# Optimization experiments

Measured on AMD Instinct MI355X. Metric: run time of the kernel, lower is better.

Reference implementation:

```python
import jax, jax.numpy as jnp
import numpy as np

HID = 128
NLAYERS = 8
LAT = 32
DIM_IN = 63 + 15 + LAT  # pe(xyz,L=10)=3+60, pe(shift,L=2)=3+12, latent=32 -> 110


def _pe(x, L):
    # NeRF positional encoding, include_input=True, freq-major [sin3,cos3] per freq
    freqs = (2.0 ** jnp.arange(L)).astype(x.dtype)
    xf = x[..., None, :] * freqs[:, None]                      # [..., L, 3]
    sc = jnp.concatenate([jnp.sin(xf), jnp.cos(xf)], axis=-1)  # [..., L, 6]
    return jnp.concatenate([x, sc.reshape(*x.shape[:-1], 6 * L)], axis=-1)


def setup_inputs() -> dict:
    key = jax.random.key(0)
    ks = jax.random.split(key, 24)
    B, P, V = 2, 32768, 5023
    d = {}
    d["pts"] = jax.random.normal(ks[0], (B, P, 3), jnp.float32)
    d["deformed_mesh_pts"] = jax.random.normal(ks[1], (B, V, 3), jnp.float32)
    d["cano_verts"] = jax.random.normal(ks[2], (1, V, 3), jnp.float32)
    d["motion_latent"] = jax.random.normal(ks[3], (B, P, LAT), jnp.float32)
    for i in range(NLAYERS):
        fin = DIM_IN if i == 0 else (DIM_IN + HID if i == NLAYERS // 2 else HID)
        d[f"w{i}"] = jax.random.normal(ks[4 + i], (HID, fin), jnp.float32) / np.sqrt(fin).astype(np.float32)
        d[f"b{i}"] = jnp.zeros((HID,), jnp.float32)
    d["w_out"] = jax.random.normal(ks[20], (3, HID), jnp.float32) * 0.01
    d["b_out"] = jnp.zeros((3,), jnp.float32)
    return d


def reference(pts, deformed_mesh_pts, cano_verts, motion_latent,
              w0, b0, w1, b1, w2, b2, w3, b3, w4, b4, w5, b5, w6, b6, w7, b7,
              w_out, b_out):
    # mesh-guided shift per vertex
    mesh_shift = cano_verts - deformed_mesh_pts                 # [B,V,3]
    # point-to-point NN search (squared euclidean cdist + argmin)
    d2 = ((pts ** 2).sum(-1)[:, :, None]
          + (deformed_mesh_pts ** 2).sum(-1)[:, None, :]
          - 2.0 * jnp.einsum('bpc,bvc->bpv', pts, deformed_mesh_pts))  # [B,P,V]
    d2 = jnp.maximum(d2, 0.0)
    idx = jnp.argmin(d2, axis=-1)                               # [B,P]
    dist = jnp.min(d2, axis=-1)                                 # [B,P]
    weight = jnp.exp(-dist)[..., None]                          # 1/exp(dist)
    gidx = jnp.broadcast_to(idx[:, :, None], idx.shape + (3,))
    gshift = jnp.take_along_axis(mesh_shift, gidx, axis=1) * weight  # [B,P,3]
    # deformation MLP with skip connection at layer 4
    initial = jnp.concatenate([_pe(pts, 10), _pe(gshift, 2), motion_latent], axis=-1)
    ws = [w0, w1, w2, w3, w4, w5, w6, w7]
    bs = [b0, b1, b2, b3, b4, b5, b6, b7]
    x = initial
    last_feat = x
    for i in range(NLAYERS):
        inp = jnp.concatenate([initial, x], axis=-1) if i == NLAYERS // 2 else x
        x = inp @ ws[i].T + bs[i]
        last_feat = x  # pre-activation feature (out_feat_ls[-1])
        x = jax.nn.relu(x)
    mlp_shift = x @ w_out.T + b_out                             # [B,P,3]
    pts_shifts = gshift + mlp_shift
    return pts + pts_shifts, last_feat
```

## Files before the change

### kernel.cpp

```cpp
#include <hip/hip_runtime.h>
#include <math.h>

typedef unsigned short ushort_t;
typedef unsigned int   uint_t;
typedef __attribute__((ext_vector_type(8)))  short bf16x8;
typedef __attribute__((ext_vector_type(16))) float f32x16;

#define NPTS   65536
#define NV     5023
#define NVP    5120
#define NTILE  160
#define HTILE  80
#define LATD   32
#define KF     110
#define FSTR   112
#define MARGIN 1.5e-2f

union U4 { uint_t u[4]; bf16x8 v; };

__device__ __forceinline__ ushort_t f2bf(float f) {
  union { float f; unsigned u; } x; x.f = f;
  unsigned r = x.u + 0x7fffu + ((x.u >> 16) & 1u);
  return (ushort_t)(r >> 16);
}
__device__ __forceinline__ float bf2f(ushort_t u) {
  union { unsigned u; float f; } x; x.u = ((unsigned)u) << 16;
  return x.f;
}
__device__ __forceinline__ uint_t packsplit(float v) {
  const ushort_t h = f2bf(v);
  const ushort_t l = f2bf(v - bf2f(h));
  return (uint_t)h | ((uint_t)l << 16);
}

__device__ __forceinline__ void dbl_step(float& s, float& c) {
  const float t = s * c;
  const float cn = fmaf(-2.f * s, s, 1.f);
  s = t + t;
  c = cn;
}

__global__ __launch_bounds__(256) void k_prep(
    const float* __restrict__ dm,
    const float* __restrict__ w0, const float* __restrict__ w1,
    const float* __restrict__ w2, const float* __restrict__ w3,
    const float* __restrict__ w4, const float* __restrict__ w5,
    const float* __restrict__ w6, const float* __restrict__ w7,
    ushort_t* __restrict__ wsWh, ushort_t* __restrict__ wsWl,
    ushort_t* __restrict__ aFF, ushort_t* __restrict__ aFH,
    float4* __restrict__ vq)
{
  const int e = blockIdx.x * 256 + threadIdx.x;
  {
    const int p = e >> 14, local = e & 16383;
    const int j   = local & 7;
    const int lh  = (local >> 3) & 1;
    const int l31 = (local >> 4) & 31;
    const int tn  = (local >> 9) & 3;
    const int ks  = (local >> 11) & 7;
    const int n = tn*32 + l31;
    const int k = ks*16 + lh*8 + j;
    float v;
    if (p == 0)      v = (k < KF) ? w0[n*110 + k] : 0.f;
    else if (p == 1) v = w1[n*128 + k];
    else if (p == 2) v = w2[n*128 + k];
    else if (p == 3) v = w3[n*128 + k];
    else if (p == 4) v = (k < KF) ? w4[n*238 + k] : 0.f;
    else if (p == 5) v = w4[n*238 + KF + k];
    else if (p == 6) v = w5[n*128 + k];
    else if (p == 7) v = w6[n*128 + k];
    else             v = w7[n*128 + k];
    const ushort_t h = f2bf(v);
    wsWh[e] = h;
    wsWl[e] = f2bf(v - bf2f(h));
  }
  if (e < 2*NVP) {
    const int b = (e >= NVP) ? 1 : 0;
    const int v = e - b*NVP;
    const float* __restrict__ dmb = dm + b*NV*3;
    float x = 0.f, y = 0.f, z = 0.f, wv = 3.0e38f;
    if (v < NV) {
      x = dmb[v*3+0]; y = dmb[v*3+1]; z = dmb[v*3+2];
      wv = fmaf(x,x, fmaf(y,y, z*z));
    }
    const ushort_t hx = f2bf(x),  hy = f2bf(y),  hz = f2bf(z),  hw = f2bf(wv);
    const ushort_t lx = f2bf(x - bf2f(hx)), ly = f2bf(y - bf2f(hy));
    const ushort_t lz = f2bf(z - bf2f(hz)), lw = f2bf(wv - bf2f(hw));
    U4 F, H;
    F.u[0] = (uint_t)hx | ((uint_t)hy << 16);
    F.u[1] = (uint_t)hz | ((uint_t)hw << 16);
    F.u[2] = (uint_t)lx | ((uint_t)ly << 16);
    F.u[3] = (uint_t)lz | ((uint_t)lw << 16);
    H.u[0] = F.u[0]; H.u[1] = F.u[1]; H.u[2] = 0; H.u[3] = 0;
    *(bf16x8*)(aFF + (size_t)e*8) = F.v;
    *(bf16x8*)(aFH + (size_t)e*8) = H.v;
    vq[e] = make_float4(x, y, z, wv);
  }
}

__device__ __forceinline__ float min16(const f32x16& d) {
  const float t0 = fminf(fminf(d[0],d[1]),   fminf(d[2],d[3]));
  const float t1 = fminf(fminf(d[4],d[5]),   fminf(d[6],d[7]));
  const float t2 = fminf(fminf(d[8],d[9]),   fminf(d[10],d[11]));
  const float t3 = fminf(fminf(d[12],d[13]), fminf(d[14],d[15]));
  return fminf(fminf(t0,t1), fminf(t2,t3));
}

__global__ __launch_bounds__(256, 4) void k_nnfeat(
    const float* __restrict__ pts, const float* __restrict__ dm,
    const float* __restrict__ cano, const float* __restrict__ lat,
    const ushort_t* __restrict__ aFF, const ushort_t* __restrict__ aFH,
    const float4* __restrict__ vq,
    uint_t* __restrict__ feat, float* __restrict__ base3)
{
  __shared__ float sMin[2][64];
  __shared__ float sDh[2][64];
  __shared__ int   sIh[2][64];

  const int tid = threadIdx.x;
  const int lane = tid & 63, w = tid >> 6;
  const int l31 = lane & 31, lh = lane >> 5;
  const int half = w & 1, pg = w >> 1;
  const int g0 = blockIdx.x * 64;
  const int b  = blockIdx.x >> 9;
  const int pt = g0 + pg*32 + l31;
  const int pidx = pg*32 + l31;

  const float px = pts[pt*3+0], py = pts[pt*3+1], pz = pts[pt*3+2];
  const float p2 = fmaf(px,px, fmaf(py,py, pz*pz));

  const float tpx = -2.f*px, tpy = -2.f*py, tpz = -2.f*pz;
  const ushort_t hpx = f2bf(tpx), hpy = f2bf(tpy), hpz = f2bf(tpz);
  const ushort_t lpx = f2bf(tpx - bf2f(hpx));
  const ushort_t lpy = f2bf(tpy - bf2f(hpy));
  const ushort_t lpz = f2bf(tpz - bf2f(hpz));
  U4 Bh, Bl;
  Bh.u[0] = (uint_t)hpx | ((uint_t)hpy << 16);
  Bh.u[1] = (uint_t)hpz | (0x3F80u << 16);
  Bh.u[2] = Bh.u[0]; Bh.u[3] = Bh.u[1];
  Bl.u[0] = (uint_t)lpx | ((uint_t)lpy << 16);
  Bl.u[1] = (uint_t)lpz;
  Bl.u[2] = 0; Bl.u[3] = 0;
  const bf16x8 bfrag = lh ? Bl.v : Bh.v;

  const ushort_t* __restrict__ aBase = (lh ? aFH : aFF)
      + (size_t)b * NVP * 8 + (size_t)half * HTILE * 32 * 8;
  const float4*   __restrict__ vqb   = vq + (size_t)b * NVP;
  const int vho = half * HTILE * 32;

  const f32x16 zacc = (f32x16)(0.f);

  float gmin = 3.0e38f;
  bf16x8 ap0, ap1, ap2, ap3, an0, an1, an2, an3;
  ap0 = *(const bf16x8*)(aBase + (size_t)(0*32 + l31)*8);
  ap1 = *(const bf16x8*)(aBase + (size_t)(1*32 + l31)*8);
  ap2 = *(const bf16x8*)(aBase + (size_t)(2*32 + l31)*8);
  ap3 = *(const bf16x8*)(aBase + (size_t)(3*32 + l31)*8);
  #pragma unroll 2
  for (int tb = 0; tb < HTILE/4; ++tb) {
    const int t0 = tb*4;
    if (tb + 1 < HTILE/4) {
      an0 = *(const bf16x8*)(aBase + (size_t)((t0+4)*32 + l31)*8);
      an1 = *(const bf16x8*)(aBase + (size_t)((t0+5)*32 + l31)*8);
      an2 = *(const bf16x8*)(aBase + (size_t)((t0+6)*32 + l31)*8);
      an3 = *(const bf16x8*)(aBase + (size_t)((t0+7)*32 + l31)*8);
    }
    const f32x16 d0 = __builtin_amdgcn_mfma_f32_32x32x16_bf16(ap0, bfrag, zacc, 0,0,0);
    const f32x16 d1 = __builtin_amdgcn_mfma_f32_32x32x16_bf16(ap1, bfrag, zacc, 0,0,0);
    const f32x16 d2 = __builtin_amdgcn_mfma_f32_32x32x16_bf16(ap2, bfrag, zacc, 0,0,0);
    const f32x16 d3 = __builtin_amdgcn_mfma_f32_32x32x16_bf16(ap3, bfrag, zacc, 0,0,0);
    const float m0 = min16(d0), m1 = min16(d1), m2 = min16(d2), m3 = min16(d3);
    gmin = fminf(gmin, fminf(fminf(m0,m1), fminf(m2,m3)));
    ap0 = an0; ap1 = an1; ap2 = an2; ap3 = an3;
  }
  gmin = fminf(gmin, __shfl_xor(gmin, 32, 64));
  if (lh == 0) sMin[half][pidx] = gmin;
  __syncthreads();
  const float thr = fminf(sMin[0][pidx], sMin[1][pidx]) + MARGIN;

  float bs = 3.4e38f; int bi = 0;
  ap0 = *(const bf16x8*)(aBase + (size_t)(0*32 + l31)*8);
  ap1 = *(const bf16x8*)(aBase + (size_t)(1*32 + l31)*8);
  ap2 = *(const bf16x8*)(aBase + (size_t)(2*32 + l31)*8);
  ap3 = *(const bf16x8*)(aBase + (size_t)(3*32 + l31)*8);
  #pragma unroll 1
  for (int tb = 0; tb < HTILE/4; ++tb) {
    const int t0 = tb*4;
    if (tb + 1 < HTILE/4) {
      an0 = *(const bf16x8*)(aBase + (size_t)((t0+4)*32 + l31)*8);
      an1 = *(const bf16x8*)(aBase + (size_t)((t0+5)*32 + l31)*8);
      an2 = *(const bf16x8*)(aBase + (size_t)((t0+6)*32 + l31)*8);
      an3 = *(const bf16x8*)(aBase + (size_t)((t0+7)*32 + l31)*8);
    }
    f32x16 dd[4];
    dd[0] = __builtin_amdgcn_mfma_f32_32x32x16_bf16(ap0, bfrag, zacc, 0,0,0);
    dd[1] = __builtin_amdgcn_mfma_f32_32x32x16_bf16(ap1, bfrag, zacc, 0,0,0);
    dd[2] = __builtin_amdgcn_mfma_f32_32x32x16_bf16(ap2, bfrag, zacc, 0,0,0);
    dd[3] = __builtin_amdgcn_mfma_f32_32x32x16_bf16(ap3, bfrag, zacc, 0,0,0);
    #pragma unroll
    for (int i = 0; i < 4; ++i) {
      const f32x16 d = dd[i];
      float q4[4];
      q4[0] = fminf(fminf(d[0],d[1]),   fminf(d[2],d[3]));
      q4[1] = fminf(fminf(d[4],d[5]),   fminf(d[6],d[7]));
      q4[2] = fminf(fminf(d[8],d[9]),   fminf(d[10],d[11]));
      q4[3] = fminf(fminf(d[12],d[13]), fminf(d[14],d[15]));
      const float tm = fminf(fminf(q4[0],q4[1]), fminf(q4[2],q4[3]));
      if (tm <= thr) {
        const int t = t0 + i;
        #pragma unroll
        for (int q = 0; q < 4; ++q) {
          if (q4[q] <= thr) {
            #pragma unroll
            for (int rr = 0; rr < 4; ++rr) {
              const int r = q*4 + rr;
              if (d[r] <= thr) {
                const int row = (r & 3) + 8*(r >> 2) + 4*lh;
                const int v = vho + t*32 + row;
                const float4 qv = vqb[v];
                const float dot = fmaf(px, qv.x, fmaf(py, qv.y, pz*qv.z));
                float d2 = fmaf(-2.f, dot, p2 + qv.w);
                d2 = fmaxf(d2, 0.f);
                if (d2 < bs || (d2 == bs && v < bi)) { bs = d2; bi = v; }
              }
            }
          }
        }
      }
    }
    ap0 = an0; ap1 = an1; ap2 = an2; ap3 = an3;
  }
  {
    const float ob = __shfl_xor(bs, 32, 64);
    const int   oi = __shfl_xor(bi, 32, 64);
    if (ob < bs || (ob == bs && oi < bi)) { bs = ob; bi = oi; }
  }
  if (lh == 0) { sDh[half][pidx] = bs; sIh[half][pidx] = bi; }
  __syncthreads();

  const int p = tid & 63, slice = tid >> 6;
  const int g = g0 + p;
  float wd = sDh[0][p]; int wi = sIh[0][p];
  {
    const float od = sDh[1][p]; const int oi = sIh[1][p];
    if (od < wd || (od == wd && oi < wi)) { wd = od; wi = oi; }
  }
  const float* __restrict__ dmb = dm + b * NV * 3;

  const float qx = pts[g*3+0], qy = pts[g*3+1], qz = pts[g*3+2];
  const float wgt = expf(-wd);
  const float sx = (cano[wi*3+0] - dmb[wi*3+0]) * wgt;
  const float sy = (cano[wi*3+1] - dmb[wi*3+1]) * wgt;
  const float sz = (cano[wi*3+2] - dmb[wi*3+2]) * wgt;

  uint_t* __restrict__ fr = feat + (size_t)g * FSTR;

  if (slice == 0) {
    base3[g*3+0] = qx + sx; base3[g*3+1] = qy + sy; base3[g*3+2] = qz + sz;
    fr[0] = packsplit(qx); fr[1] = packsplit(qy); fr[2] = packsplit(qz);
    float s0,c0,s1,c1,s2,c2;
    sincosf(qx,&s0,&c0); sincosf(qy,&s1,&c1); sincosf(qz,&s2,&c2);
    #pragma unroll
    for (int f = 0; f < 3; ++f) {
      const int k = 3 + 6*f;
      fr[k+0]=packsplit(s0); fr[k+1]=packsplit(s1); fr[k+2]=packsplit(s2);
      fr[k+3]=packsplit(c0); fr[k+4]=packsplit(c1); fr[k+5]=packsplit(c2);
      if (f < 2) { dbl_step(s0,c0); dbl_step(s1,c1); dbl_step(s2,c2); }
    }
    fr[110] = 0; fr[111] = 0;
  } else if (slice == 1) {
    float s0,c0,s1,c1,s2,c2;
    sincosf(qx*8.f,&s0,&c0); sincosf(qy*8.f,&s1,&c1); sincosf(qz*8.f,&s2,&c2);
    #pragma unroll
    for (int f = 3; f < 7; ++f) {
      const int k = 3 + 6*f;
      fr[k+0]=packsplit(s0); fr[k+1]=packsplit(s1); fr[k+2]=packsplit(s2);
      fr[k+3]=packsplit(c0); fr[k+4]=packsplit(c1); fr[k+5]=packsplit(c2);
      if (f < 6) { dbl_step(s0,c0); dbl_step(s1,c1); dbl_step(s2,c2); }
    }
  } else if (slice == 2) {
    float s0,c0,s1,c1,s2,c2;
    sincosf(qx*128.f,&s0,&c0); sincosf(qy*128.f,&s1,&c1); sincosf(qz*128.f,&s2,&c2);
    #pragma unroll
    for (int f = 7; f < 10; ++f) {
      const int k = 3 + 6*f;
      fr[k+0]=packsplit(s0); fr[k+1]=packsplit(s1); fr[k+2]=packsplit(s2);
      fr[k+3]=packsplit(c0); fr[k+4]=packsplit(c1); fr[k+5]=packsplit(c2);
      if (f < 9) { dbl_step(s0,c0); dbl_step(s1,c1); dbl_step(s2,c2); }
    }
    #pragma unroll
    for (int j = 0; j < 16; ++j) fr[78+j] = packsplit(lat[g*LATD + j]);
  } else {
    fr[63]=packsplit(sx); fr[64]=packsplit(sy); fr[65]=packsplit(sz);
    float s0,c0,s1,c1,s2,c2;
    sincosf(sx,&s0,&c0); sincosf(sy,&s1,&c1); sincosf(sz,&s2,&c2);
    #pragma unroll
    for (int f = 0; f < 2; ++f) {
      const int k = 66 + 6*f;
      fr[k+0]=packsplit(s0); fr[k+1]=packsplit(s1); fr[k+2]=packsplit(s2);
      fr[k+3]=packsplit(c0); fr[k+4]=packsplit(c1); fr[k+5]=packsplit(c2);
      if (f < 1) { dbl_step(s0,c0); dbl_step(s1,c1); dbl_step(s2,c2); }
    }
    #pragma unroll
    for (int j = 16; j < 32; ++j) fr[78+j] = packsplit(lat[g*LATD + j]);
  }
}


__device__ __forceinline__ void zero4(f32x16 (&a)[4]) {
  #pragma unroll
  for (int i = 0; i < 4; ++i) a[i] = (f32x16)(0.f);
}

__device__ __forceinline__ void load_feat_frags(
    const uint_t* __restrict__ fr, bf16x8 (&Xh)[8], bf16x8 (&Xl)[8], int lh)
{
  #pragma unroll
  for (int ks = 0; ks < 7; ++ks) {
    const int k0 = ks*16 + lh*8;
    const uint4 ua = *(const uint4*)(fr + k0);
    const uint4 ub = *(const uint4*)(fr + k0 + 4);
    U4 H, L;
    H.u[0] = (ua.x & 0xffffu) | (ua.y << 16);
    H.u[1] = (ua.z & 0xffffu) | (ua.w << 16);
    H.u[2] = (ub.x & 0xffffu) | (ub.y << 16);
    H.u[3] = (ub.z & 0xffffu) | (ub.w << 16);
    L.u[0] = (ua.x >> 16) | (ua.y & 0xffff0000u);
    L.u[1] = (ua.z >> 16) | (ua.w & 0xffff0000u);
    L.u[2] = (ub.x >> 16) | (ub.y & 0xffff0000u);
    L.u[3] = (ub.z >> 16) | (ub.w & 0xffff0000u);
    Xh[ks] = H.v; Xl[ks] = L.v;
  }
}

__device__ __forceinline__ void load_slab(bf16x8 (&wh)[4], bf16x8 (&wl)[4],
    const ushort_t* __restrict__ Wh, const ushort_t* __restrict__ Wl,
    int ks, int l31, int lh)
{
  const int lo = l31*16 + lh*8;
  #pragma unroll
  for (int tn = 0; tn < 4; ++tn) {
    const int off = (ks*4 + tn)*512 + lo;
    wh[tn] = *(const bf16x8*)(Wh + off);
    wl[tn] = *(const bf16x8*)(Wl + off);
  }
}

__device__ __forceinline__ void mfma_slab(f32x16 (&acc)[4],
    const bf16x8 (&wh)[4], const bf16x8 (&wl)[4],
    const bf16x8& xh, const bf16x8& xl)
{
  #pragma unroll
  for (int tn = 0; tn < 4; ++tn) {
    acc[tn] = __builtin_amdgcn_mfma_f32_32x32x16_bf16(wh[tn], xh, acc[tn], 0,0,0);
    acc[tn] = __builtin_amdgcn_mfma_f32_32x32x16_bf16(wl[tn], xh, acc[tn], 0,0,0);
    acc[tn] = __builtin_amdgcn_mfma_f32_32x32x16_bf16(wh[tn], xl, acc[tn], 0,0,0);
  }
}

template<int NKS, bool TAIL>
__device__ __forceinline__ void run_panel(f32x16 (&acc)[4],
    const ushort_t* __restrict__ Wh, const ushort_t* __restrict__ Wl,
    const ushort_t* __restrict__ WhN, const ushort_t* __restrict__ WlN,
    bf16x8 (&wbh)[2][4], bf16x8 (&wbl)[2][4],
    const bf16x8 (&Xh)[8], const bf16x8 (&Xl)[8], int l31, int lh)
{
  #pragma unroll
  for (int ks = 0; ks < NKS; ++ks) {
    const int b = ks & 1;
    mfma_slab(acc, wbh[b], wbl[b], Xh[ks], Xl[ks]);
    if (ks + 2 < NKS) {
      load_slab(wbh[b], wbl[b], Wh, Wl, ks + 2, l31, lh);
    } else if (TAIL) {
      load_slab(wbh[b], wbl[b], WhN, WlN, ks & 1, l31, lh);
    }
  }
}

__device__ __forceinline__ void bias_relu(f32x16 (&acc)[4],
    const float* __restrict__ bias, int lh)
{
  #pragma unroll
  for (int tn = 0; tn < 4; ++tn)
    #pragma unroll
    for (int b = 0; b < 4; ++b) {
      const float4 b4 = *(const float4*)(bias + tn*32 + 8*b + 4*lh);
      acc[tn][4*b+0] = fmaxf(acc[tn][4*b+0] + b4.x, 0.f);
      acc[tn][4*b+1] = fmaxf(acc[tn][4*b+1] + b4.y, 0.f);
      acc[tn][4*b+2] = fmaxf(acc[tn][4*b+2] + b4.z, 0.f);
      acc[tn][4*b+3] = fmaxf(acc[tn][4*b+3] + b4.w, 0.f);
    }
}

__device__ __forceinline__ void build_frags(const f32x16 (&acc)[4],
    bf16x8 (&Xh)[8], bf16x8 (&Xl)[8], int lh)
{
  #pragma unroll
  for (int ks = 0; ks < 8; ++ks) {
    const int tn = ks >> 1;
    const int rb = 8*(ks & 1);
    const float f0 = acc[tn][rb+0], f1 = acc[tn][rb+1];
    const float f2 = acc[tn][rb+2], f3 = acc[tn][rb+3];
    const float f4 = acc[tn][rb+4], f5 = acc[tn][rb+5];
    const float f6 = acc[tn][rb+6], f7 = acc[tn][rb+7];
    const ushort_t h0=f2bf(f0), h1=f2bf(f1), h2=f2bf(f2), h3=f2bf(f3);
    const ushort_t h4=f2bf(f4), h5=f2bf(f5), h6=f2bf(f6), h7=f2bf(f7);
    const uint_t hA0 = (uint_t)h0 | ((uint_t)h1 << 16);
    const uint_t hA1 = (uint_t)h2 | ((uint_t)h3 << 16);
    const uint_t hB0 = (uint_t)h4 | ((uint_t)h5 << 16);
    const uint_t hB1 = (uint_t)h6 | ((uint_t)h7 << 16);
    const uint_t lA0 = (uint_t)f2bf(f0 - bf2f(h0)) | ((uint_t)f2bf(f1 - bf2f(h1)) << 16);
    const uint_t lA1 = (uint_t)f2bf(f2 - bf2f(h2)) | ((uint_t)f2bf(f3 - bf2f(h3)) << 16);
    const uint_t lB0 = (uint_t)f2bf(f4 - bf2f(h4)) | ((uint_t)f2bf(f5 - bf2f(h5)) << 16);
    const uint_t lB1 = (uint_t)f2bf(f6 - bf2f(h6)) | ((uint_t)f2bf(f7 - bf2f(h7)) << 16);
    const uint_t sh0 = lh ? hA0 : hB0, sh1 = lh ? hA1 : hB1;
    const uint_t sl0 = lh ? lA0 : lB0, sl1 = lh ? lA1 : lB1;
    const uint_t rh0 = __shfl_xor(sh0, 32, 64), rh1 = __shfl_xor(sh1, 32, 64);
    const uint_t rl0 = __shfl_xor(sl0, 32, 64), rl1 = __shfl_xor(sl1, 32, 64);
    U4 H, L;
    H.u[0] = lh ? rh0 : hA0;  H.u[1] = lh ? rh1 : hA1;
    H.u[2] = lh ? hB0 : rh0;  H.u[3] = lh ? hB1 : rh1;
    L.u[0] = lh ? rl0 : lA0;  L.u[1] = lh ? rl1 : lA1;
    L.u[2] = lh ? lB0 : rl0;  L.u[3] = lh ? lB1 : rl1;
    Xh[ks] = H.v; Xl[ks] = L.v;
  }
}

__global__ __launch_bounds__(256, 2) void k_mlp(
    const uint_t* __restrict__ feat, const float* __restrict__ base3,
    const ushort_t* __restrict__ wsWh, const ushort_t* __restrict__ wsWl,
    const float* __restrict__ b0, const float* __restrict__ b1,
    const float* __restrict__ b2, const float* __restrict__ b3,
    const float* __restrict__ b4, const float* __restrict__ b5,
    const float* __restrict__ b6, const float* __restrict__ b7,
    const float* __restrict__ w_out, const float* __restrict__ b_out,
    float* __restrict__ out)
{
  __shared__ __align__(16) float sF[4][32*132];
  __shared__ __align__(16) float sB[8*128 + 384 + 4];

  const int tid  = threadIdx.x;
  const int lane = tid & 63, wid = tid >> 6;
  const int l31 = lane & 31, lh = lane >> 5;
  const int p0 = blockIdx.x * 128 + wid * 32;

  {
    const float* bsp[8] = {b0,b1,b2,b3,b4,b5,b6,b7};
    if (tid < 128) {
      #pragma unroll
      for (int l = 0; l < 8; ++l) sB[l*128 + tid] = bsp[l][tid];
    }
    for (int i = tid; i < 384; i += 256) sB[1024 + i] = w_out[i];
    if (tid < 3) sB[1408 + tid] = b_out[tid];
  }

  const uint_t* __restrict__ fr = feat + (size_t)(p0 + l31) * FSTR;

  bf16x8 Xh[8], Xl[8];
  bf16x8 wbh[2][4], wbl[2][4];
  f32x16 acc[4];

  load_slab(wbh[0], wbl[0], wsWh, wsWl, 0, l31, lh);
  load_slab(wbh[1], wbl[1], wsWh, wsWl, 1, l31, lh);
  load_feat_frags(fr, Xh, Xl, lh);
  __syncthreads();

  zero4(acc);
  run_panel<7,true>(acc, wsWh + 0*16384, wsWl + 0*16384,
                         wsWh + 1*16384, wsWl + 1*16384, wbh, wbl, Xh, Xl, l31, lh);
  bias_relu(acc, sB + 0*128, lh);
  build_frags(acc, Xh, Xl, lh);

  zero4(acc);
  run_panel<8,true>(acc, wsWh + 1*16384, wsWl + 1*16384,
                         wsWh + 2*16384, wsWl + 2*16384, wbh, wbl, Xh, Xl, l31, lh);
  bias_relu(acc, sB + 1*128, lh);
  build_frags(acc, Xh, Xl, lh);

  zero4(acc);
  run_panel<8,true>(acc, wsWh + 2*16384, wsWl + 2*16384,
                         wsWh + 3*16384, wsWl + 3*16384, wbh, wbl, Xh, Xl, l31, lh);
  bias_relu(acc, sB + 2*128, lh);
  build_frags(acc, Xh, Xl, lh);

  zero4(acc);
  run_panel<8,true>(acc, wsWh + 3*16384, wsWl + 3*16384,
                         wsWh + 5*16384, wsWl + 5*16384, wbh, wbl, Xh, Xl, l31, lh);
  bias_relu(acc, sB + 3*128, lh);
  build_frags(acc, Xh, Xl, lh);

  zero4(acc);
  run_panel<8,true>(acc, wsWh + 5*16384, wsWl + 5*16384,
                         wsWh + 4*16384, wsWl + 4*16384, wbh, wbl, Xh, Xl, l31, lh);
  load_feat_frags(fr, Xh, Xl, lh);
  run_panel<7,true>(acc, wsWh + 4*16384, wsWl + 4*16384,
                         wsWh + 6*16384, wsWl + 6*16384, wbh, wbl, Xh, Xl, l31, lh);
  bias_relu(acc, sB + 4*128, lh);
  build_frags(acc, Xh, Xl, lh);

  zero4(acc);
  run_panel<8,true>(acc, wsWh + 6*16384, wsWl + 6*16384,
                         wsWh + 7*16384, wsWl + 7*16384, wbh, wbl, Xh, Xl, l31, lh);
  bias_relu(acc, sB + 5*128, lh);
  build_frags(acc, Xh, Xl, lh);

  zero4(acc);
  run_panel<8,true>(acc, wsWh + 7*16384, wsWl + 7*16384,
                         wsWh + 8*16384, wsWl + 8*16384, wbh, wbl, Xh, Xl, l31, lh);
  bias_relu(acc, sB + 6*128, lh);
  build_frags(acc, Xh, Xl, lh);

  zero4(acc);
  run_panel<8,false>(acc, wsWh + 8*16384, wsWl + 8*16384,
                          (const ushort_t*)0, (const ushort_t*)0, wbh, wbl, Xh, Xl, l31, lh);

  float* __restrict__ sFw = &sF[wid][0];
  #pragma unroll
  for (int tn = 0; tn < 4; ++tn)
    #pragma unroll
    for (int b = 0; b < 4; ++b) {
      const int n0 = tn*32 + 8*b + 4*lh;
      const float4 bv = *(const float4*)(sB + 7*128 + n0);
      const float v0 = acc[tn][4*b+0] + bv.x;
      const float v1 = acc[tn][4*b+1] + bv.y;
      const float v2 = acc[tn][4*b+2] + bv.z;
      const float v3 = acc[tn][4*b+3] + bv.w;
      *(float4*)(sFw + l31*132 + n0) = make_float4(v0, v1, v2, v3);
      acc[tn][4*b+0] = fmaxf(v0, 0.f);
      acc[tn][4*b+1] = fmaxf(v1, 0.f);
      acc[tn][4*b+2] = fmaxf(v2, 0.f);
      acc[tn][4*b+3] = fmaxf(v3, 0.f);
    }

  asm volatile("s_waitcnt lgkmcnt(0)" ::: "memory");
  __builtin_amdgcn_sched_barrier(0);

  float* __restrict__ out1 = out + (size_t)NPTS * 3;
  #pragma unroll
  for (int i = 0; i < 16; ++i) {
    const int idx = i*64 + lane;
    const int p = idx >> 5, q = idx & 31;
    const float4 v = *(const float4*)(sFw + p*132 + q*4);
    *(float4*)(out1 + (size_t)(p0 + p)*128 + q*4) = v;
  }

  float dotc[3];
  #pragma unroll
  for (int c = 0; c < 3; ++c) {
    float a = 0.f;
    #pragma unroll
    for (int tn = 0; tn < 4; ++tn)
      #pragma unroll
      for (int b = 0; b < 4; ++b) {
        const int n0 = tn*32 + 8*b + 4*lh;
        const float4 w4 = *(const float4*)(sB + 1024 + c*128 + n0);
        a = fmaf(acc[tn][4*b+0], w4.x, a);
        a = fmaf(acc[tn][4*b+1], w4.y, a);
        a = fmaf(acc[tn][4*b+2], w4.z, a);
        a = fmaf(acc[tn][4*b+3], w4.w, a);
      }
    a += __shfl_xor(a, 32, 64);
    dotc[c] = a;
  }
  if (lh == 0) {
    const int g = p0 + l31;
    #pragma unroll
    for (int c = 0; c < 3; ++c)
      out[g*3 + c] = base3[g*3 + c] + dotc[c] + sB[1408 + c];
  }
}

extern "C" void kernel_launch(void* const* d_in, const int* in_sizes, int n_in,
                              void* d_out, int out_size, void* d_ws, size_t ws_size,
                              hipStream_t stream)
{
  const float* pts  = (const float*)d_in[0];
  const float* dm   = (const float*)d_in[1];
  const float* cano = (const float*)d_in[2];
  const float* lat  = (const float*)d_in[3];
  const float* w[8]; const float* b[8];
  for (int i = 0; i < 8; ++i) {
    w[i] = (const float*)d_in[4 + 2*i];
    b[i] = (const float*)d_in[5 + 2*i];
  }
  const float* w_out = (const float*)d_in[20];
  const float* b_out = (const float*)d_in[21];
  float* out = (float*)d_out;

  uint_t*   feat  = (uint_t*)d_ws;
  float*    base3 = (float*)((char*)d_ws + (size_t)NPTS*FSTR*4);
  ushort_t* wsWh  = (ushort_t*)((char*)base3 + (size_t)NPTS*3*4);
  ushort_t* wsWl  = wsWh + 147456;
  ushort_t* aFF   = wsWl + 147456;
  ushort_t* aFH   = aFF + 2*NVP*8;
  float4*   vq    = (float4*)(aFH + 2*NVP*8);

  k_prep<<<576, 256, 0, stream>>>(dm,
      w[0],w[1],w[2],w[3],w[4],w[5],w[6],w[7], wsWh, wsWl, aFF, aFH, vq);
  k_nnfeat<<<1024, 256, 0, stream>>>(pts, dm, cano, lat, aFF, aFH, vq, feat, base3);
  k_mlp<<<NPTS/128, 256, 0, stream>>>(feat, base3, wsWh, wsWl,
      b[0],b[1],b[2],b[3],b[4],b[5],b[6],b[7], w_out, b_out, out);
}
```

Baseline: 232.1 us.

## Split NN vertex scan across four waves per 32-point block, doubling grid

Each block now handles 32 points instead of 64, with its four waves each scanning a quarter of the vertex tiles instead of two waves per half. Partial minima and argmins are merged through shared memory over four slots. The feature-writing epilogue is spread over eight 32-thread slices, with latent packing split into four slices. Launch bounds ask for 8 blocks per CU and the grid doubles to 2048. The aim is shorter per-wave serial scans and more parallelism, at the cost of more block overhead and more pressure on registers to reach the higher occupancy target.

```diff
diff --git a/kernel.cpp b/kernel.cpp
--- a/kernel.cpp
+++ b/kernel.cpp
@@ -10,7 +10,7 @@
 #define NV     5023
 #define NVP    5120
 #define NTILE  160
-#define HTILE  80
+#define QTILE  40
 #define LATD   32
 #define KF     110
 #define FSTR   112
@@ -106,25 +106,23 @@
   return fminf(fminf(t0,t1), fminf(t2,t3));
 }
 
-__global__ __launch_bounds__(256, 4) void k_nnfeat(
+__global__ __launch_bounds__(256, 8) void k_nnfeat(
     const float* __restrict__ pts, const float* __restrict__ dm,
     const float* __restrict__ cano, const float* __restrict__ lat,
     const ushort_t* __restrict__ aFF, const ushort_t* __restrict__ aFH,
     const float4* __restrict__ vq,
     uint_t* __restrict__ feat, float* __restrict__ base3)
 {
-  __shared__ float sMin[2][64];
-  __shared__ float sDh[2][64];
-  __shared__ int   sIh[2][64];
+  __shared__ float sMin[4][32];
+  __shared__ float sDh[4][32];
+  __shared__ int   sIh[4][32];
 
   const int tid = threadIdx.x;
   const int lane = tid & 63, w = tid >> 6;
   const int l31 = lane & 31, lh = lane >> 5;
-  const int half = w & 1, pg = w >> 1;
-  const int g0 = blockIdx.x * 64;
-  const int b  = blockIdx.x >> 9;
-  const int pt = g0 + pg*32 + l31;
-  const int pidx = pg*32 + l31;
+  const int g0 = blockIdx.x * 32;
+  const int b  = blockIdx.x >> 10;
+  const int pt = g0 + l31;
 
   const float px = pts[pt*3+0], py = pts[pt*3+1], pz = pts[pt*3+2];
   const float p2 = fmaf(px,px, fmaf(py,py, pz*pz));
@@ -144,9 +142,9 @@
   const bf16x8 bfrag = lh ? Bl.v : Bh.v;
 
   const ushort_t* __restrict__ aBase = (lh ? aFH : aFF)
-      + (size_t)b * NVP * 8 + (size_t)half * HTILE * 32 * 8;
+      + (size_t)b * NVP * 8 + (size_t)w * QTILE * 32 * 8;
   const float4*   __restrict__ vqb   = vq + (size_t)b * NVP;
-  const int vho = half * HTILE * 32;
+  const int vho = w * QTILE * 32;
 
   const f32x16 zacc = (f32x16)(0.f);
 
@@ -157,9 +155,9 @@
   ap2 = *(const bf16x8*)(aBase + (size_t)(2*32 + l31)*8);
   ap3 = *(const bf16x8*)(aBase + (size_t)(3*32 + l31)*8);
   #pragma unroll 2
-  for (int tb = 0; tb < HTILE/4; ++tb) {
+  for (int tb = 0; tb < QTILE/4; ++tb) {
     const int t0 = tb*4;
-    if (tb + 1 < HTILE/4) {
+    if (tb + 1 < QTILE/4) {
       an0 = *(const bf16x8*)(aBase + (size_t)((t0+4)*32 + l31)*8);
       an1 = *(const bf16x8*)(aBase + (size_t)((t0+5)*32 + l31)*8);
       an2 = *(const bf16x8*)(aBase + (size_t)((t0+6)*32 + l31)*8);
@@ -174,9 +172,10 @@
     ap0 = an0; ap1 = an1; ap2 = an2; ap3 = an3;
   }
   gmin = fminf(gmin, __shfl_xor(gmin, 32, 64));
-  if (lh == 0) sMin[half][pidx] = gmin;
+  if (lane < 32) sMin[w][l31] = gmin;
   __syncthreads();
-  const float thr = fminf(sMin[0][pidx], sMin[1][pidx]) + MARGIN;
+  const float thr = fminf(fminf(sMin[0][l31], sMin[1][l31]),
+                          fminf(sMin[2][l31], sMin[3][l31])) + MARGIN;
 
   float bs = 3.4e38f; int bi = 0;
   ap0 = *(const bf16x8*)(aBase + (size_t)(0*32 + l31)*8);
@@ -184,9 +183,9 @@
   ap2 = *(const bf16x8*)(aBase + (size_t)(2*32 + l31)*8);
   ap3 = *(const bf16x8*)(aBase + (size_t)(3*32 + l31)*8);
   #pragma unroll 1
-  for (int tb = 0; tb < HTILE/4; ++tb) {
+  for (int tb = 0; tb < QTILE/4; ++tb) {
     const int t0 = tb*4;
-    if (tb + 1 < HTILE/4) {
+    if (tb + 1 < QTILE/4) {
       an0 = *(const bf16x8*)(aBase + (size_t)((t0+4)*32 + l31)*8);
       an1 = *(const bf16x8*)(aBase + (size_t)((t0+5)*32 + l31)*8);
       an2 = *(const bf16x8*)(aBase + (size_t)((t0+6)*32 + l31)*8);
@@ -235,14 +234,15 @@
     const int   oi = __shfl_xor(bi, 32, 64);
     if (ob < bs || (ob == bs && oi < bi)) { bs = ob; bi = oi; }
   }
-  if (lh == 0) { sDh[half][pidx] = bs; sIh[half][pidx] = bi; }
+  if (lane < 32) { sDh[w][l31] = bs; sIh[w][l31] = bi; }
   __syncthreads();
 
-  const int p = tid & 63, slice = tid >> 6;
+  const int p = tid & 31, slice = tid >> 5;
   const int g = g0 + p;
   float wd = sDh[0][p]; int wi = sIh[0][p];
-  {
-    const float od = sDh[1][p]; const int oi = sIh[1][p];
+  #pragma unroll
+  for (int qq = 1; qq < 4; ++qq) {
+    const float od = sDh[qq][p]; const int oi = sIh[qq][p];
     if (od < wd || (od == wd && oi < wi)) { wd = od; wi = oi; }
   }
   const float* __restrict__ dmb = dm + b * NV * 3;
@@ -267,7 +267,6 @@
       fr[k+3]=packsplit(c0); fr[k+4]=packsplit(c1); fr[k+5]=packsplit(c2);
       if (f < 2) { dbl_step(s0,c0); dbl_step(s1,c1); dbl_step(s2,c2); }
     }
-    fr[110] = 0; fr[111] = 0;
   } else if (slice == 1) {
     float s0,c0,s1,c1,s2,c2;
     sincosf(qx*8.f,&s0,&c0); sincosf(qy*8.f,&s1,&c1); sincosf(qz*8.f,&s2,&c2);
@@ -288,9 +287,7 @@
       fr[k+3]=packsplit(c0); fr[k+4]=packsplit(c1); fr[k+5]=packsplit(c2);
       if (f < 9) { dbl_step(s0,c0); dbl_step(s1,c1); dbl_step(s2,c2); }
     }
-    #pragma unroll
-    for (int j = 0; j < 16; ++j) fr[78+j] = packsplit(lat[g*LATD + j]);
-  } else {
+  } else if (slice == 3) {
     fr[63]=packsplit(sx); fr[64]=packsplit(sy); fr[65]=packsplit(sz);
     float s0,c0,s1,c1,s2,c2;
     sincosf(sx,&s0,&c0); sincosf(sy,&s1,&c1); sincosf(sz,&s2,&c2);
@@ -301,8 +298,11 @@
       fr[k+3]=packsplit(c0); fr[k+4]=packsplit(c1); fr[k+5]=packsplit(c2);
       if (f < 1) { dbl_step(s0,c0); dbl_step(s1,c1); dbl_step(s2,c2); }
     }
-    #pragma unroll
-    for (int j = 16; j < 32; ++j) fr[78+j] = packsplit(lat[g*LATD + j]);
+    fr[110] = 0; fr[111] = 0;
+  } else {
+    const int j0 = (slice - 4) * 8;
+    #pragma unroll
+    for (int j = 0; j < 8; ++j) fr[78 + j0 + j] = packsplit(lat[g*LATD + j0 + j]);
   }
 }
 
@@ -597,7 +597,7 @@
 
   k_prep<<<576, 256, 0, stream>>>(dm,
       w[0],w[1],w[2],w[3],w[4],w[5],w[6],w[7], wsWh, wsWl, aFF, aFH, vq);
-  k_nnfeat<<<1024, 256, 0, stream>>>(pts, dm, cano, lat, aFF, aFH, vq, feat, base3);
+  k_nnfeat<<<2048, 256, 0, stream>>>(pts, dm, cano, lat, aFF, aFH, vq, feat, base3);
   k_mlp<<<NPTS/128, 256, 0, stream>>>(feat, base3, wsWh, wsWl,
       b[0],b[1],b[2],b[3],b[4],b[5],b[6],b[7], w_out, b_out, out);
 }
```

Result: slower. 785.7 us (+238.5%).
